# Performance work log

Measured on AMD Instinct MI355X. Metric: run time of the kernel, lower is better.

Reference implementation:

```python
import jax, jax.numpy as jnp
import numpy as np

B, T, D, H = 4, 2048, 1024, 16
DK = D // H

def setup_inputs() -> dict:
    key = jax.random.key(0)
    k1, k2, k3 = jax.random.split(key, 3)
    s = 1.0 / np.sqrt(D)
    return {
        "x": jax.random.normal(k1, (B, T, D), dtype=jnp.float32),
        "W_qkv": jax.random.normal(k2, (D, 3 * D), dtype=jnp.float32) * s,
        "b_qkv": jnp.zeros((3 * D,), dtype=jnp.float32),
        "W_out": jax.random.normal(k3, (D, D), dtype=jnp.float32) * s,
        "b_out": jnp.zeros((D,), dtype=jnp.float32),
    }

def reference(x, W_qkv, b_qkv, W_out, b_out):
    Bx, Tx, C = x.shape
    qkv = x @ W_qkv + b_qkv                       # [B,T,3D]
    q, k, v = jnp.split(qkv, 3, axis=-1)
    # [B,T,D] -> [B,H,T,dk]
    def heads(t):
        return t.reshape(Bx, Tx, H, DK).transpose(0, 2, 1, 3)
    q, k, v = heads(q), heads(k), heads(v)
    scores = jnp.einsum('bhqd,bhkd->bhqk', q, k) / jnp.sqrt(jnp.float32(DK))
    causal = jnp.tril(jnp.ones((Tx, Tx), dtype=bool))  # [T,T]
    scores = jnp.where(causal[None, None], scores, -jnp.inf)
    attn = jax.nn.softmax(scores, axis=-1)        # dropout p=0 (eval)
    out = jnp.einsum('bhqk,bhkd->bhqd', attn, v)  # [B,H,T,dk]
    out = out.transpose(0, 2, 1, 3).reshape(Bx, Tx, C)
    return out @ W_out + b_out
```

## Files before the change

### kernel.cpp

```cpp
#include <hip/hip_runtime.h>
#include <hip/hip_bf16.h>
#include <stdint.h>

#define T_SEQ 2048
#define DMODEL 1024
#define NH 16
#define DKH 64
#define M_TOK 8192
#define N_QKV 3072
#define K_DIM 1024

#define ATTN_SC (0.125f * 1.44269504f)

typedef __attribute__((ext_vector_type(8))) short short8;
typedef __attribute__((ext_vector_type(4))) short short4v;
typedef __attribute__((ext_vector_type(4))) float float4v;
typedef __attribute__((ext_vector_type(2))) unsigned int uint2v;

__device__ inline short bf16_bits(float f) {
  __hip_bfloat16 h = __float2bfloat16(f);
  short s;
  __builtin_memcpy(&s, &h, 2);
  return s;
}

__device__ inline short4v pack4_bf16_fast(float a, float b, float c, float d) {
  unsigned ua = __builtin_bit_cast(unsigned, a) + 0x8000u;
  unsigned ub = __builtin_bit_cast(unsigned, b) + 0x8000u;
  unsigned uc = __builtin_bit_cast(unsigned, c) + 0x8000u;
  unsigned ud = __builtin_bit_cast(unsigned, d) + 0x8000u;
  uint2v uu = {(ua >> 16) | (ub & 0xFFFF0000u),
               (uc >> 16) | (ud & 0xFFFF0000u)};
  return __builtin_bit_cast(short4v, uu);
}

__device__ inline short4v pack4_bf16_trunc(float a, float b, float c, float d) {
  unsigned ua = __builtin_bit_cast(unsigned, a);
  unsigned ub = __builtin_bit_cast(unsigned, b);
  unsigned uc = __builtin_bit_cast(unsigned, c);
  unsigned ud = __builtin_bit_cast(unsigned, d);
  uint2v uu = {__builtin_amdgcn_perm(ub, ua, 0x07060302u),
               __builtin_amdgcn_perm(ud, uc, 0x07060302u)};
  return __builtin_bit_cast(short4v, uu);
}

__device__ inline void async_load16(const void* g, void* l) {
  __builtin_amdgcn_global_load_lds(
      (const __attribute__((address_space(1))) unsigned int*)g,
      (__attribute__((address_space(3))) unsigned int*)l,
      16, 0, 0);
}


__global__ __launch_bounds__(256) void cvt_kernel(const float* __restrict__ in,
                                                  short* __restrict__ out, int n) {
  int idx = (blockIdx.x * 256 + threadIdx.x) * 4;
  if (idx < n) {
    float4v v = *(const float4v*)(in + idx);
    short4v o;
    o[0] = bf16_bits(v[0]); o[1] = bf16_bits(v[1]);
    o[2] = bf16_bits(v[2]); o[3] = bf16_bits(v[3]);
    *(short4v*)(out + idx) = o;
  }
}

__global__ __launch_bounds__(256) void transpose_cvt(const float* __restrict__ in,
                                                     short* __restrict__ out,
                                                     int K, int N) {
  __shared__ float tile[32][33];
  int n0 = blockIdx.x * 32, k0 = blockIdx.y * 32;
  int tx = threadIdx.x, ty = threadIdx.y;
  #pragma unroll
  for (int r = ty; r < 32; r += 8)
    tile[r][tx] = in[(size_t)(k0 + r) * N + n0 + tx];
  __syncthreads();
  #pragma unroll
  for (int r = ty; r < 32; r += 8)
    out[(size_t)(n0 + r) * K + k0 + tx] = bf16_bits(tile[tx][r]);
}


template <int EPI>
__global__ __launch_bounds__(256) void gemm_bt(
    const short* __restrict__ A, const short* __restrict__ Bt,
    const float* __restrict__ bias,
    short* __restrict__ Qb, short* __restrict__ Kf, short* __restrict__ Vf,
    float* __restrict__ Cout, int M, int N, int K, int ntile0) {
  constexpr bool CT = (EPI != 1);
  __shared__ __align__(16) short AsB[3][128 * 32];
  __shared__ __align__(16) short BsB[3][128 * 32];
  const int tid = threadIdx.x;
  const int lane = tid & 63;
  const int wave = tid >> 6;
  const int m0 = blockIdx.x * 128;
  const int n0 = (blockIdx.y + ntile0) * 128;
  const int wm = (wave >> 1) * 64;
  const int wn = (wave & 1) * 64;
  const int quad = lane >> 4;
  const int l16 = lane & 15;

  float4v acc[4][4] = {};

  const int r0 = tid >> 2, r1 = r0 + 64;
  const int oswz = (((tid & 3) - (tid >> 3)) & 3) * 8;
  const int lo0 = wave * 512;
  const int lo1 = 2048 + wave * 512;

  const short* Ag0 = A  + (size_t)(m0 + r0) * K + oswz;
  const short* Ag1 = A  + (size_t)(m0 + r1) * K + oswz;
  const short* Bg0 = Bt + (size_t)(n0 + r0) * K + oswz;
  const short* Bg1 = Bt + (size_t)(n0 + r1) * K + oswz;

  const int sw = ((quad + (l16 >> 1)) & 3) * 8;

  auto stage = [&](int t, int b) {
    const int kt = t << 5;
    async_load16(Ag0 + kt, &AsB[b][0] + lo0);
    async_load16(Ag1 + kt, &AsB[b][0] + lo1);
    async_load16(Bg0 + kt, &BsB[b][0] + lo0);
    async_load16(Bg1 + kt, &BsB[b][0] + lo1);
  };

  const int nkt = K >> 5;
  stage(0, 0);
  stage(1, 1);

  int c0 = 0, c1 = 1, c2 = 2;
  for (int it = 0; it < nkt; ++it) {
    if (it < nkt - 1)
      __builtin_amdgcn_s_waitcnt(0x0F74);
    else
      __builtin_amdgcn_s_waitcnt(0x0F70);
    __builtin_amdgcn_s_barrier();
    __builtin_amdgcn_sched_barrier(0);
    if (it + 2 < nkt) stage(it + 2, c2);

    const short* As = &AsB[c0][0];
    const short* Bs = &BsB[c0][0];
    short8 af[4], bfr[4];
    #pragma unroll
    for (int t = 0; t < 4; ++t)
      af[t] = *(const short8*)(As + (size_t)(wm + t * 16 + l16) * 32 + sw);
    #pragma unroll
    for (int t = 0; t < 4; ++t)
      bfr[t] = *(const short8*)(Bs + (size_t)(wn + t * 16 + l16) * 32 + sw);
    #pragma unroll
    for (int i = 0; i < 4; ++i)
      #pragma unroll
      for (int j = 0; j < 4; ++j) {
        if (CT)
          acc[i][j] = __builtin_amdgcn_mfma_f32_16x16x32_bf16(bfr[j], af[i], acc[i][j], 0, 0, 0);
        else
          acc[i][j] = __builtin_amdgcn_mfma_f32_16x16x32_bf16(af[i], bfr[j], acc[i][j], 0, 0, 0);
      }

    const int tr = c0; c0 = c1; c1 = c2; c2 = tr;
  }

  if (EPI == 0) {
    const int which = n0 >> 10;
    #pragma unroll
    for (int tj = 0; tj < 4; ++tj) {
      const int colb = n0 + wn + tj * 16 + quad * 4;
      float4v bz = *(const float4v*)(bias + colb);
      const int d = colb & 1023;
      const int h = d >> 6, dkb = d & 63;
      #pragma unroll
      for (int ti = 0; ti < 4; ++ti) {
        const int tok = m0 + wm + ti * 16 + l16;
        const int b = tok >> 11, t = tok & 2047;
        const size_t bhoff = (size_t)(b * NH + h) * (T_SEQ * DKH);
        float4v v = acc[ti][tj];
        if (which == 0) {
          short4v o = pack4_bf16_fast((v[0] + bz[0]) * ATTN_SC, (v[1] + bz[1]) * ATTN_SC,
                                      (v[2] + bz[2]) * ATTN_SC, (v[3] + bz[3]) * ATTN_SC);
          *(short4v*)(Qb + bhoff + (size_t)t * DKH + dkb) = o;
        } else {
          short4v o = pack4_bf16_fast(v[0] + bz[0], v[1] + bz[1], v[2] + bz[2], v[3] + bz[3]);
          const int h2 = dkb >> 5, qd = (dkb >> 3) & 3, w = dkb & 7;
          size_t kbase = bhoff + (size_t)(t >> 6) * 4096 +
                         ((((t >> 4) & 3) * 2 + h2) * 4 + qd) * 128 + (t & 15) * 8 + w;
          *(short4v*)(Kf + kbase) = o;
        }
      }
    }
  } else if (EPI == 1) {
    #pragma unroll
    for (int tj = 0; tj < 4; ++tj) {
      const int col = n0 + wn + tj * 16 + l16;
      const float bz = bias[col];
      const int d = col & 1023;
      const int h = d >> 6, dk = d & 63;
      #pragma unroll
      for (int ti = 0; ti < 4; ++ti) {
        const int rbase = m0 + wm + ti * 16 + quad * 4;
        const int b = rbase >> 11, t = rbase & 2047;
        const size_t bhoff = (size_t)(b * NH + h) * (T_SEQ * DKH);
        float4v v = acc[ti][tj];
        short4v pv = pack4_bf16_fast(v[0] + bz, v[1] + bz, v[2] + bz, v[3] + bz);
        size_t off = bhoff + (size_t)(t >> 6) * 4096 +
                     ((((t >> 4) & 3) * 4 + (dk >> 4)) * 4 + ((t >> 2) & 3)) * 64 +
                     (dk & 15) * 4;
        *(short4v*)(Vf + off) = pv;
      }
    }
  } else {
    #pragma unroll
    for (int tj = 0; tj < 4; ++tj) {
      const int colb = n0 + wn + tj * 16 + quad * 4;
      float4v bz = *(const float4v*)(bias + colb);
      #pragma unroll
      for (int ti = 0; ti < 4; ++ti) {
        const int row = m0 + wm + ti * 16 + l16;
        float4v v = acc[ti][tj];
        float4v o = {v[0] + bz[0], v[1] + bz[1], v[2] + bz[2], v[3] + bz[3]};
        *(float4v*)(Cout + (size_t)row * N + colb) = o;
      }
    }
  }
}


template <int MASK>
__device__ __forceinline__ void attn_tile(
    const short* __restrict__ Ks, const short* __restrict__ Vs,
    const short8 aq[2][2], short4v ones,
    float4v oc[2][4], float4v lc[2],
    int dkq, int quad, int l16) {
  const int mb = dkq + quad * 4 - l16;
  #pragma unroll
  for (int c = 0; c < 4; ++c) {
    short8 b0 = *(const short8*)(Ks + (c * 2 + 0) * 512 + quad * 128 + l16 * 8);
    short8 b1 = *(const short8*)(Ks + (c * 2 + 1) * 512 + quad * 128 + l16 * 8);
    short4v vf[4];
    #pragma unroll
    for (int d = 0; d < 4; ++d)
      vf[d] = *(const short4v*)(Vs + (c * 4 + d) * 256 + quad * 64 + l16 * 4);
    #pragma unroll
    for (int qi = 0; qi < 2; ++qi) {
      float4v z = {0.f, 0.f, 0.f, 0.f};
      z = __builtin_amdgcn_mfma_f32_16x16x32_bf16(b0, aq[qi][0], z, 0, 0, 0);
      z = __builtin_amdgcn_mfma_f32_16x16x32_bf16(b1, aq[qi][1], z, 0, 0, 0);
      float p[4];
      #pragma unroll
      for (int i = 0; i < 4; ++i) {
        p[i] = __builtin_amdgcn_exp2f(z[i]);
        if (MASK && (mb + c * 16 + i - qi * 16 > 0)) p[i] = 0.f;
      }
      short4v pb = pack4_bf16_trunc(p[0], p[1], p[2], p[3]);
      lc[qi] = __builtin_amdgcn_mfma_f32_16x16x16bf16_1k(ones, pb, lc[qi], 0, 0, 0);
      #pragma unroll
      for (int d = 0; d < 4; ++d)
        oc[qi][d] = __builtin_amdgcn_mfma_f32_16x16x16bf16_1k(vf[d], pb, oc[qi][d], 0, 0, 0);
    }
  }
}

__global__ __launch_bounds__(256) void attn_kernel(const short* __restrict__ Qb,
                                                   const short* __restrict__ Kf,
                                                   const short* __restrict__ Vf,
                                                   short* __restrict__ Ao) {
  __shared__ __align__(16) short KsB[2][4096];
  __shared__ __align__(16) short VsB[2][4096];
  const int bh = blockIdx.x;
  const int y = blockIdx.y;
  const int qb = (y < 4) ? (15 - y) : (y < 8) ? (y - 4) : (y < 12) ? (19 - y) : (y - 8);
  const int tid = threadIdx.x;
  const int lane = tid & 63, wave = tid >> 6;
  const int quad = lane >> 4, l16 = lane & 15;
  const int qw0 = qb * 128 + wave * 32;
  const int nkb = 2 * qb + 2;

  const short* Qg = Qb + ((size_t)bh * T_SEQ + qw0) * DKH;
  const short* Kg0 = Kf + (size_t)bh * (T_SEQ * DKH);
  const short* Vg0 = Vf + (size_t)bh * (T_SEQ * DKH);

  short8 aq[2][2];
  #pragma unroll
  for (int qi = 0; qi < 2; ++qi)
    #pragma unroll
    for (int h = 0; h < 2; ++h)
      aq[qi][h] = *(const short8*)(Qg + (size_t)(qi * 16 + l16) * DKH + h * 32 + quad * 8);

  float4v oc[2][4] = {};
  float4v lc[2] = {};
  short4v ones = {0x3F80, 0x3F80, 0x3F80, 0x3F80};

  async_load16(Kg0 + tid * 8,        &KsB[0][0] + wave * 512);
  async_load16(Kg0 + 2048 + tid * 8, &KsB[0][0] + 2048 + wave * 512);
  async_load16(Vg0 + tid * 8,        &VsB[0][0] + wave * 512);
  async_load16(Vg0 + 2048 + tid * 8, &VsB[0][0] + 2048 + wave * 512);

  for (int kb = 0; kb < nkb; ++kb) {
    __builtin_amdgcn_s_waitcnt(0);
    __syncthreads();

    if (kb + 1 < nkb) {
      const int nb = (kb + 1) & 1;
      const short* Kg = Kg0 + (size_t)(kb + 1) * 4096;
      const short* Vg = Vg0 + (size_t)(kb + 1) * 4096;
      async_load16(Kg + tid * 8,        &KsB[nb][0] + wave * 512);
      async_load16(Kg + 2048 + tid * 8, &KsB[nb][0] + 2048 + wave * 512);
      async_load16(Vg + tid * 8,        &VsB[nb][0] + wave * 512);
      async_load16(Vg + 2048 + tid * 8, &VsB[nb][0] + 2048 + wave * 512);
    }

    const int dkq = kb * 64 - qw0;
    if (dkq + 63 <= 0) {
      attn_tile<0>(&KsB[kb & 1][0], &VsB[kb & 1][0], aq, ones, oc, lc, dkq, quad, l16);
    } else if (dkq <= 31) {
      attn_tile<1>(&KsB[kb & 1][0], &VsB[kb & 1][0], aq, ones, oc, lc, dkq, quad, l16);
    }
  }

  const int b = bh >> 4, h = bh & 15;
  #pragma unroll
  for (int qi = 0; qi < 2; ++qi) {
    float rl = 1.0f / lc[qi][0];
    #pragma unroll
    for (int d = 0; d < 4; ++d) {
      short4v o;
      #pragma unroll
      for (int i = 0; i < 4; ++i) o[i] = bf16_bits(oc[qi][d][i] * rl);
      int t = qw0 + qi * 16 + l16;
      *(short4v*)(Ao + (size_t)(b * T_SEQ + t) * DMODEL + h * DKH + d * 16 + quad * 4) = o;
    }
  }
}


extern "C" void kernel_launch(void* const* d_in, const int* in_sizes, int n_in,
                              void* d_out, int out_size, void* d_ws, size_t ws_size,
                              hipStream_t stream) {
  const float* x    = (const float*)d_in[0];
  const float* Wqkv = (const float*)d_in[1];
  const float* bqkv = (const float*)d_in[2];
  const float* Wout = (const float*)d_in[3];
  const float* bout = (const float*)d_in[4];
  float* out = (float*)d_out;

  char* ws = (char*)d_ws;
  short* Xb    = (short*)(ws);
  short* Wqkvt = (short*)(ws + (16ull << 20));
  short* Woutt = (short*)(ws + (22ull << 20));
  short* Qb    = (short*)(ws + (24ull << 20));
  short* Kf    = (short*)(ws + (40ull << 20));
  short* Vf    = (short*)(ws + (56ull << 20));
  short* Ao    = (short*)(ws + (72ull << 20));

  cvt_kernel<<<(M_TOK * K_DIM / 4 + 255) / 256, 256, 0, stream>>>(x, Xb, M_TOK * K_DIM);
  dim3 tb(32, 8);
  transpose_cvt<<<dim3(N_QKV / 32, K_DIM / 32), tb, 0, stream>>>(Wqkv, Wqkvt, K_DIM, N_QKV);
  transpose_cvt<<<dim3(DMODEL / 32, K_DIM / 32), tb, 0, stream>>>(Wout, Woutt, K_DIM, DMODEL);

  gemm_bt<0><<<dim3(M_TOK / 128, 16), 256, 0, stream>>>(
      Xb, Wqkvt, bqkv, Qb, Kf, nullptr, nullptr, M_TOK, N_QKV, K_DIM, 0);
  gemm_bt<1><<<dim3(M_TOK / 128, 8), 256, 0, stream>>>(
      Xb, Wqkvt, bqkv, nullptr, nullptr, Vf, nullptr, M_TOK, N_QKV, K_DIM, 16);

  attn_kernel<<<dim3(64, T_SEQ / 128), 256, 0, stream>>>(Qb, Kf, Vf, Ao);

  gemm_bt<2><<<dim3(M_TOK / 128, DMODEL / 128), 256, 0, stream>>>(
      Ao, Woutt, bout, nullptr, nullptr, nullptr, out, M_TOK, DMODEL, K_DIM, 0);
}
```

Measured before the change: 254.5 us.

## Use 256x128 GEMM tiles with 512 threads and merge QKV launches

The GEMM tile grows from 128x128 to 256x128 with 8 waves per block, so each B tile loaded into shared memory is reused across twice as many rows. The two QKV launches become one kernel that branches on the column tile to choose the Q/K or V epilogue. MFMA sections are also wrapped in s_setprio to raise wave priority during compute. Shared memory per block grows to about 72KB and the grid has half as many blocks, which risks lower occupancy or poorer wave balance across CUs.

```diff
diff --git a/kernel.cpp b/kernel.cpp
--- a/kernel.cpp
+++ b/kernel.cpp
@@ -80,55 +80,44 @@
 }
 
 
-template <int EPI>
-__global__ __launch_bounds__(256) void gemm_bt(
+template <bool CT>
+__device__ __forceinline__ void gemm_core256(
     const short* __restrict__ A, const short* __restrict__ Bt,
-    const float* __restrict__ bias,
-    short* __restrict__ Qb, short* __restrict__ Kf, short* __restrict__ Vf,
-    float* __restrict__ Cout, int M, int N, int K, int ntile0) {
-  constexpr bool CT = (EPI != 1);
-  __shared__ __align__(16) short AsB[3][128 * 32];
-  __shared__ __align__(16) short BsB[3][128 * 32];
-  const int tid = threadIdx.x;
+    int m0, int n0, int tid,
+    short (&AsB)[3][8192], short (&BsB)[3][4096],
+    float4v (&acc)[4][4]) {
   const int lane = tid & 63;
   const int wave = tid >> 6;
-  const int m0 = blockIdx.x * 128;
-  const int n0 = (blockIdx.y + ntile0) * 128;
   const int wm = (wave >> 1) * 64;
   const int wn = (wave & 1) * 64;
   const int quad = lane >> 4;
   const int l16 = lane & 15;
 
-  float4v acc[4][4] = {};
-
-  const int r0 = tid >> 2, r1 = r0 + 64;
+  const int r0 = tid >> 2;
   const int oswz = (((tid & 3) - (tid >> 3)) & 3) * 8;
-  const int lo0 = wave * 512;
-  const int lo1 = 2048 + wave * 512;
-
-  const short* Ag0 = A  + (size_t)(m0 + r0) * K + oswz;
-  const short* Ag1 = A  + (size_t)(m0 + r1) * K + oswz;
-  const short* Bg0 = Bt + (size_t)(n0 + r0) * K + oswz;
-  const short* Bg1 = Bt + (size_t)(n0 + r1) * K + oswz;
+  const int lo = wave * 512;
+
+  const short* Ag0 = A  + (size_t)(m0 + r0) * K_DIM + oswz;
+  const short* Ag1 = A  + (size_t)(m0 + r0 + 128) * K_DIM + oswz;
+  const short* Bg0 = Bt + (size_t)(n0 + r0) * K_DIM + oswz;
 
   const int sw = ((quad + (l16 >> 1)) & 3) * 8;
 
   auto stage = [&](int t, int b) {
     const int kt = t << 5;
-    async_load16(Ag0 + kt, &AsB[b][0] + lo0);
-    async_load16(Ag1 + kt, &AsB[b][0] + lo1);
-    async_load16(Bg0 + kt, &BsB[b][0] + lo0);
-    async_load16(Bg1 + kt, &BsB[b][0] + lo1);
+    async_load16(Ag0 + kt, &AsB[b][0] + lo);
+    async_load16(Ag1 + kt, &AsB[b][0] + 4096 + lo);
+    async_load16(Bg0 + kt, &BsB[b][0] + lo);
   };
 
-  const int nkt = K >> 5;
+  const int nkt = K_DIM >> 5;
   stage(0, 0);
   stage(1, 1);
 
   int c0 = 0, c1 = 1, c2 = 2;
   for (int it = 0; it < nkt; ++it) {
-    if (it < nkt - 1)
-      __builtin_amdgcn_s_waitcnt(0x0F74);
+    if (it + 1 < nkt)
+      __builtin_amdgcn_s_waitcnt(0x0F73);
     else
       __builtin_amdgcn_s_waitcnt(0x0F70);
     __builtin_amdgcn_s_barrier();
@@ -144,6 +133,7 @@
     #pragma unroll
     for (int t = 0; t < 4; ++t)
       bfr[t] = *(const short8*)(Bs + (size_t)(wn + t * 16 + l16) * 32 + sw);
+    __builtin_amdgcn_s_setprio(1);
     #pragma unroll
     for (int i = 0; i < 4; ++i)
       #pragma unroll
@@ -153,11 +143,33 @@
         else
           acc[i][j] = __builtin_amdgcn_mfma_f32_16x16x32_bf16(af[i], bfr[j], acc[i][j], 0, 0, 0);
       }
+    __builtin_amdgcn_s_setprio(0);
 
     const int tr = c0; c0 = c1; c1 = c2; c2 = tr;
   }
-
-  if (EPI == 0) {
+}
+
+
+__global__ __launch_bounds__(512, 2) void gemm_qkv(
+    const short* __restrict__ A, const short* __restrict__ Bt,
+    const float* __restrict__ bias,
+    short* __restrict__ Qb, short* __restrict__ Kf, short* __restrict__ Vf) {
+  __shared__ __align__(16) short AsB[3][8192];
+  __shared__ __align__(16) short BsB[3][4096];
+  const int tid = threadIdx.x;
+  const int lane = tid & 63;
+  const int wave = tid >> 6;
+  const int m0 = blockIdx.x * 256;
+  const int n0 = blockIdx.y * 128;
+  const int wm = (wave >> 1) * 64;
+  const int wn = (wave & 1) * 64;
+  const int quad = lane >> 4;
+  const int l16 = lane & 15;
+
+  float4v acc[4][4] = {};
+
+  if (n0 < 2048) {
+    gemm_core256<true>(A, Bt, m0, n0, tid, AsB, BsB, acc);
     const int which = n0 >> 10;
     #pragma unroll
     for (int tj = 0; tj < 4; ++tj) {
@@ -184,7 +196,8 @@
         }
       }
     }
-  } else if (EPI == 1) {
+  } else {
+    gemm_core256<false>(A, Bt, m0, n0, tid, AsB, BsB, acc);
     #pragma unroll
     for (int tj = 0; tj < 4; ++tj) {
       const int col = n0 + wn + tj * 16 + l16;
@@ -204,18 +217,38 @@
         *(short4v*)(Vf + off) = pv;
       }
     }
-  } else {
-    #pragma unroll
-    for (int tj = 0; tj < 4; ++tj) {
-      const int colb = n0 + wn + tj * 16 + quad * 4;
-      float4v bz = *(const float4v*)(bias + colb);
-      #pragma unroll
-      for (int ti = 0; ti < 4; ++ti) {
-        const int row = m0 + wm + ti * 16 + l16;
-        float4v v = acc[ti][tj];
-        float4v o = {v[0] + bz[0], v[1] + bz[1], v[2] + bz[2], v[3] + bz[3]};
-        *(float4v*)(Cout + (size_t)row * N + colb) = o;
-      }
+  }
+}
+
+
+__global__ __launch_bounds__(512, 2) void gemm_out(
+    const short* __restrict__ A, const short* __restrict__ Bt,
+    const float* __restrict__ bias, float* __restrict__ Cout) {
+  __shared__ __align__(16) short AsB[3][8192];
+  __shared__ __align__(16) short BsB[3][4096];
+  const int tid = threadIdx.x;
+  const int lane = tid & 63;
+  const int wave = tid >> 6;
+  const int m0 = blockIdx.x * 256;
+  const int n0 = blockIdx.y * 128;
+  const int wm = (wave >> 1) * 64;
+  const int wn = (wave & 1) * 64;
+  const int quad = lane >> 4;
+  const int l16 = lane & 15;
+
+  float4v acc[4][4] = {};
+  gemm_core256<true>(A, Bt, m0, n0, tid, AsB, BsB, acc);
+
+  #pragma unroll
+  for (int tj = 0; tj < 4; ++tj) {
+    const int colb = n0 + wn + tj * 16 + quad * 4;
+    float4v bz = *(const float4v*)(bias + colb);
+    #pragma unroll
+    for (int ti = 0; ti < 4; ++ti) {
+      const int row = m0 + wm + ti * 16 + l16;
+      float4v v = acc[ti][tj];
+      float4v o = {v[0] + bz[0], v[1] + bz[1], v[2] + bz[2], v[3] + bz[3]};
+      *(float4v*)(Cout + (size_t)row * DMODEL + colb) = o;
     }
   }
 }
@@ -353,13 +386,11 @@
   transpose_cvt<<<dim3(N_QKV / 32, K_DIM / 32), tb, 0, stream>>>(Wqkv, Wqkvt, K_DIM, N_QKV);
   transpose_cvt<<<dim3(DMODEL / 32, K_DIM / 32), tb, 0, stream>>>(Wout, Woutt, K_DIM, DMODEL);
 
-  gemm_bt<0><<<dim3(M_TOK / 128, 16), 256, 0, stream>>>(
-      Xb, Wqkvt, bqkv, Qb, Kf, nullptr, nullptr, M_TOK, N_QKV, K_DIM, 0);
-  gemm_bt<1><<<dim3(M_TOK / 128, 8), 256, 0, stream>>>(
-      Xb, Wqkvt, bqkv, nullptr, nullptr, Vf, nullptr, M_TOK, N_QKV, K_DIM, 16);
+  gemm_qkv<<<dim3(M_TOK / 256, N_QKV / 128), 512, 0, stream>>>(
+      Xb, Wqkvt, bqkv, Qb, Kf, Vf);
 
   attn_kernel<<<dim3(64, T_SEQ / 128), 256, 0, stream>>>(Qb, Kf, Vf, Ao);
 
-  gemm_bt<2><<<dim3(M_TOK / 128, DMODEL / 128), 256, 0, stream>>>(
-      Ao, Woutt, bout, nullptr, nullptr, nullptr, out, M_TOK, DMODEL, K_DIM, 0);
-}
+  gemm_out<<<dim3(M_TOK / 256, DMODEL / 128), 512, 0, stream>>>(
+      Ao, Woutt, bout, out);
+}
```

Result: no change. 252.3 us (-0.9%).
